# Kernel optimization log

Measured on AMD Instinct MI355X. Metric: run time of the kernel, lower is better.

Reference implementation:

```python
import jax, jax.numpy as jnp
import numpy as np

N = 200000
E = 6400000


def setup_inputs() -> dict:
    key = jax.random.key(0)
    k1, k2, k3, k4 = jax.random.split(key, 4)
    x = jax.random.normal(k1, (N, 10), dtype=jnp.float32)
    edge_index = jax.random.randint(k2, (2, E), 0, N, dtype=jnp.int64)
    W1 = jax.random.normal(k3, (10, 16), dtype=jnp.float32) * (1.0 / np.sqrt(10))
    b1 = jnp.zeros((16,), dtype=jnp.float32)
    W2 = jax.random.normal(k4, (16, 2), dtype=jnp.float32) * (1.0 / np.sqrt(16))
    b2 = jnp.zeros((2,), dtype=jnp.float32)
    return {"x": x, "edge_index": edge_index, "W1": W1, "b1": b1, "W2": W2, "b2": b2}


def gcn_layer(x, src, dst, W, b, num_nodes):
    # GCNConv: out = D^{-1/2} (A + I) D^{-1/2} (x W) + b, deg computed on A+I
    loop = jnp.arange(num_nodes, dtype=src.dtype)
    s = jnp.concatenate([src, loop])
    d = jnp.concatenate([dst, loop])
    deg = jax.ops.segment_sum(jnp.ones(s.shape[0], dtype=x.dtype), d, num_segments=num_nodes)
    dinv = jnp.where(deg > 0, jax.lax.rsqrt(deg), 0.0)
    norm = dinv[s] * dinv[d]                      # [E+N]
    h = x @ W                                     # [N, out] (transform before gather)
    msg = h[s] * norm[:, None]                    # [E+N, out]
    return jax.ops.segment_sum(msg, d, num_segments=num_nodes) + b


def reference(x, edge_index, W1, b1, W2, b2):
    src, dst = edge_index[0], edge_index[1]
    n = x.shape[0]
    h = jax.nn.relu(gcn_layer(x, src, dst, W1, b1, n))
    return gcn_layer(h, src, dst, W2, b2, n)
```

## Files before the change

kernel.cpp:

```cpp
#include <hip/hip_runtime.h>
#include <hip/hip_fp16.h>

#define BLK 256
#define BBLK 512
#define ABLK 512
#define DBLK 512
#define NBK 782
#define BW 256
#define NK2 512
#define NPAD (NBK * BW)
#define HALF (NPAD / 2)
#define CAP 8960
#define NCH 3
#define CHUNK 6144


__global__ void k_hist(const int* __restrict__ dst, int e, int* __restrict__ gcnt,
                       int* __restrict__ blockhist) {
  __shared__ int h[NBK];
  for (int i = threadIdx.x; i < NBK; i += BLK) h[i] = 0;
  __syncthreads();
  int base = blockIdx.x * CHUNK;
  int m = min(CHUNK, e - base);
  int m4 = m >> 2;
  const int4* d4 = (const int4*)(dst + base);
  for (int k = threadIdx.x; k < m4; k += BLK) {
    int4 vv = d4[k];
    atomicAdd(&h[vv.x >> 8], 1);
    atomicAdd(&h[vv.y >> 8], 1);
    atomicAdd(&h[vv.z >> 8], 1);
    atomicAdd(&h[vv.w >> 8], 1);
  }
  for (int k = (m4 << 2) + threadIdx.x; k < m; k += BLK)
    atomicAdd(&h[dst[base + k] >> 8], 1);
  __syncthreads();
  int* row = blockhist + (size_t)blockIdx.x * NBK;
  int sft = (blockIdx.x * 193) % NBK;
  for (int bb = threadIdx.x; bb < NBK; bb += BLK) {
    int b = bb + sft; if (b >= NBK) b -= NBK;
    int c = h[b];
    row[b] = c;
    if (c) atomicAdd(&gcnt[b], c);
  }
}

__global__ void k_scan(const int* __restrict__ gcnt, int* __restrict__ gbase,
                       int* __restrict__ gcur, int e) {
  __shared__ int s[1024];
  int t = threadIdx.x;
  int v = (t < NBK) ? gcnt[t] : 0;
  s[t] = v;
  __syncthreads();
  for (int d = 1; d < 1024; d <<= 1) {
    int u = (t >= d) ? s[t - d] : 0;
    __syncthreads();
    s[t] += u;
    __syncthreads();
  }
  if (t < NBK) { int ex = s[t] - v; gbase[t] = ex; gcur[t] = ex; }
  if (t == 0) gbase[NBK] = e;
}

__global__ void __launch_bounds__(BBLK) k_bin(const int* __restrict__ src,
                                              const int* __restrict__ dst, int e,
                                              int* __restrict__ gcur,
                                              const int* __restrict__ blockhist,
                                              unsigned* __restrict__ binned) {
  __shared__ int lcnt[NBK];
  __shared__ int loff[NBK + 1];
  __shared__ int lbase[NBK];
  __shared__ int wsum[8];
  __shared__ unsigned sorted[CHUNK];
  __shared__ unsigned short bkt16[CHUNK];
  int t = threadIdx.x;
  int base = blockIdx.x * CHUNK;
  int m = min(CHUNK, e - base);

  const int* row = blockhist + (size_t)blockIdx.x * NBK;
  for (int i = t; i < NBK; i += BBLK) lcnt[i] = row[i];
  __syncthreads();
  int b0 = 2 * t;
  int s0 = (b0 + 0 < NBK) ? lcnt[b0 + 0] : 0;
  int s1 = (b0 + 1 < NBK) ? lcnt[b0 + 1] : 0;
  int tsum = s0 + s1;
  int lane = t & 63, wid = t >> 6;
  int incl = tsum;
#pragma unroll
  for (int d = 1; d < 64; d <<= 1) {
    int u = __shfl_up(incl, d);
    if (lane >= d) incl += u;
  }
  if (lane == 63) wsum[wid] = incl;
  __syncthreads();
  if (t == 0) {
    int run = 0;
#pragma unroll
    for (int i = 0; i < 8; i++) { int tv = wsum[i]; wsum[i] = run; run += tv; }
  }
  __syncthreads();
  int ex = incl - tsum + wsum[wid];
  if (b0 + 0 < NBK) loff[b0 + 0] = ex;
  if (b0 + 1 < NBK) loff[b0 + 1] = ex + s0;
  if (t == 0) loff[NBK] = m;
  __syncthreads();
  int sft = (blockIdx.x * 193) % NBK;
  for (int bb = t; bb < NBK; bb += BBLK) {
    int b = bb + sft; if (b >= NBK) b -= NBK;
    int c = lcnt[b];
    lbase[b] = c ? atomicAdd(&gcur[b], c) : 0;
  }
  __syncthreads();
  for (int b = t; b < NBK; b += BBLK) lcnt[b] = loff[b];
  __syncthreads();
  for (int k = t; k < m; k += BBLK) {
    int d = dst[base + k];
    int b = d >> 8;
    int dl = d & 255;
    int pos = atomicAdd(&lcnt[b], 1);
    sorted[pos] = (unsigned)src[base + k] | ((unsigned)dl << 18);
    bkt16[pos] = (unsigned short)b;
  }
  __syncthreads();
  for (int i = t; i < m; i += BBLK) {
    int b = bkt16[i];
    binned[lbase[b] + (i - loff[b])] = sorted[i];
  }
}

__global__ void __launch_bounds__(DBLK) k_ldeg_t1(const unsigned* __restrict__ binned,
                                                  const int* __restrict__ gbase,
                                                  const float* __restrict__ x,
                                                  const float* __restrict__ W1,
                                                  int* __restrict__ deg2,
                                                  float* __restrict__ dinv,
                                                  __half* __restrict__ hs1, int n) {
  __shared__ int cnt[2][NK2];
  __shared__ float w[160];
  int t = threadIdx.x;
  cnt[0][t] = 0;
  cnt[1][t] = 0;
  if (t < 160) w[t] = W1[t];
  __syncthreads();
  int b = blockIdx.x;
  int p0 = gbase[b], p1 = gbase[b + 1];
  int h = t >> 8;
#define KEYOF(u) ((int)(((u) >> 18) << 1) | (int)(((u) & 0x3FFFFu) >= (unsigned)HALF))
  int p = p0 + t;
  for (; p + 3 * DBLK < p1; p += 4 * DBLK) {
    unsigned u0 = binned[p];
    unsigned u1 = binned[p + DBLK];
    unsigned u2 = binned[p + 2 * DBLK];
    unsigned u3 = binned[p + 3 * DBLK];
    atomicAdd(&cnt[h][KEYOF(u0)], 1);
    atomicAdd(&cnt[h][KEYOF(u1)], 1);
    atomicAdd(&cnt[h][KEYOF(u2)], 1);
    atomicAdd(&cnt[h][KEYOF(u3)], 1);
  }
  for (; p < p1; p += DBLK) {
    unsigned u = binned[p];
    atomicAdd(&cnt[h][KEYOF(u)], 1);
  }
#undef KEYOF
  __syncthreads();
  deg2[(size_t)b * NK2 + t] = cnt[0][t] + cnt[1][t];
  if (t >= BW) return;
  int v = b * BW + t;
  if (v >= n) return;
  int dg = cnt[0][2 * t] + cnt[0][2 * t + 1] + cnt[1][2 * t] + cnt[1][2 * t + 1];
  float di = rsqrtf((float)dg + 1.0f);
  dinv[v] = di;
  float xi[10];
#pragma unroll
  for (int k = 0; k < 10; k++) xi[k] = x[(size_t)v * 10 + k];
  __half2 hv[8];
#pragma unroll
  for (int j = 0; j < 8; j++) {
    float acc0 = 0.f, acc1 = 0.f;
#pragma unroll
    for (int k = 0; k < 10; k++) {
      acc0 = fmaf(xi[k], w[k * 16 + 2 * j], acc0);
      acc1 = fmaf(xi[k], w[k * 16 + 2 * j + 1], acc1);
    }
    hv[j] = __floats2half2_rn(acc0 * di, acc1 * di);
  }
  float4* o = (float4*)(hs1 + (size_t)v * 16);
  o[0] = *(float4*)&hv[0];
  o[1] = *(float4*)&hv[4];
}

__global__ void __launch_bounds__(ABLK) k_agg1s(unsigned* __restrict__ binned,
                                                const int* __restrict__ gbase,
                                                const int* __restrict__ deg2,
                                                int* __restrict__ doff,
                                                const __half* __restrict__ hs1,
                                                const float* __restrict__ dinv,
                                                const float* __restrict__ b1,
                                                const float* __restrict__ W2,
                                                float* __restrict__ hs2, int n) {
  __shared__ int cnt[NK2];
  __shared__ int off[NK2 + 1];
  __shared__ int sorted[CAP];
  __shared__ int wsum[8];
  __shared__ float w2[32];
  __shared__ float sb1[16];
  int t = threadIdx.x;
  if (t < 32) w2[t] = W2[t];
  if (t >= 32 && t < 48) sb1[t - 32] = b1[t - 32];
  int bkt = blockIdx.x;
  int p0 = gbase[bkt], p1 = gbase[bkt + 1];
  const bool fast = (p1 - p0) <= CAP;
  const int j = t >> 1;
  const int c = t & 1;
  const int lane = t & 63, wid = t >> 6;
  float acc[8];
#pragma unroll
  for (int q = 0; q < 8; q++) acc[q] = 0.f;

#define ACCR(R) { const __half2* h2_ = (const __half2*)&R; \
    float2 f0_ = __half22float2(h2_[0]); \
    float2 f1_ = __half22float2(h2_[1]); \
    float2 f2_ = __half22float2(h2_[2]); \
    float2 f3_ = __half22float2(h2_[3]); \
    acc[0] += f0_.x; acc[1] += f0_.y; acc[2] += f1_.x; acc[3] += f1_.y; \
    acc[4] += f2_.x; acc[5] += f2_.y; acc[6] += f3_.x; acc[7] += f3_.y; }

  int p = p0;
  int cidx = 0;
  while (p < p1) {
    int m = min(CAP, p1 - p);
    int myv;
    if (fast) {
      myv = deg2[(size_t)bkt * NK2 + t];
    } else {
      cnt[t] = 0;
      __syncthreads();
      for (int i = t; i < m; i += ABLK) {
        unsigned u = __builtin_nontemporal_load(&binned[p + i]);
        int key = (int)((u >> 18) << 1) | (int)((u & 0x3FFFFu) >= (unsigned)HALF);
        atomicAdd(&cnt[key], 1);
      }
      __syncthreads();
      myv = cnt[t];
    }
    int incl = myv;
#pragma unroll
    for (int d = 1; d < 64; d <<= 1) {
      int u = __shfl_up(incl, d);
      if (lane >= d) incl += u;
    }
    if (lane == 63) wsum[wid] = incl;
    __syncthreads();
    if (t == 0) {
      int run = 0;
#pragma unroll
      for (int i = 0; i < 8; i++) { int tv = wsum[i]; wsum[i] = run; run += tv; }
    }
    __syncthreads();
    int ex = incl - myv + wsum[wid];
    off[t] = ex;
    if (t == NK2 - 1) off[NK2] = m;
    cnt[t] = ex;
    __syncthreads();
    if (cidx < NCH && t <= BW) doff[((size_t)bkt * NCH + cidx) * (BW + 1) + t] = off[2 * t];
    for (int i = t; i < m; i += ABLK) {
      unsigned pk = __builtin_nontemporal_load(&binned[p + i]);
      int srcv = (int)(pk & 0x3FFFFu);
      int key = (int)((pk >> 18) << 1) | (int)(srcv >= HALF);
      int pos = atomicAdd(&cnt[key], 1);
      sorted[pos] = srcv;
    }
    __syncthreads();
    for (int i = t; i < m; i += ABLK)
      __builtin_nontemporal_store((unsigned)sorted[i], &binned[p + i]);
    int iA0 = off[2 * j], iA1 = off[2 * j + 1], iB1 = off[2 * j + 2];
    int i = iA0;
    for (; i + 3 < iA1; i += 4) {
      int s0 = sorted[i + 0];
      int s1 = sorted[i + 1];
      int s2 = sorted[i + 2];
      int s3 = sorted[i + 3];
      float4 r0 = *(const float4*)(hs1 + (size_t)s0 * 16 + c * 8);
      float4 r1 = *(const float4*)(hs1 + (size_t)s1 * 16 + c * 8);
      float4 r2 = *(const float4*)(hs1 + (size_t)s2 * 16 + c * 8);
      float4 r3 = *(const float4*)(hs1 + (size_t)s3 * 16 + c * 8);
      ACCR(r0); ACCR(r1); ACCR(r2); ACCR(r3);
    }
    for (; i < iA1; i++) {
      float4 r = *(const float4*)(hs1 + (size_t)sorted[i] * 16 + c * 8);
      ACCR(r);
    }
    __syncthreads();
    for (; i + 3 < iB1; i += 4) {
      int s0 = sorted[i + 0];
      int s1 = sorted[i + 1];
      int s2 = sorted[i + 2];
      int s3 = sorted[i + 3];
      float4 r0 = *(const float4*)(hs1 + (size_t)s0 * 16 + c * 8);
      float4 r1 = *(const float4*)(hs1 + (size_t)s1 * 16 + c * 8);
      float4 r2 = *(const float4*)(hs1 + (size_t)s2 * 16 + c * 8);
      float4 r3 = *(const float4*)(hs1 + (size_t)s3 * 16 + c * 8);
      ACCR(r0); ACCR(r1); ACCR(r2); ACCR(r3);
    }
    for (; i < iB1; i++) {
      float4 r = *(const float4*)(hs1 + (size_t)sorted[i] * 16 + c * 8);
      ACCR(r);
    }
    __syncthreads();
    p += m;
    cidx++;
  }
#undef ACCR

  int v = bkt * BW + j;
  if (v < n) {
    float di = dinv[v];
    float4 sf = *(const float4*)(hs1 + (size_t)v * 16 + c * 8);
    const __half2* sh = (const __half2*)&sf;
    float h0c = 0.f, h1c = 0.f;
#pragma unroll
    for (int q = 0; q < 4; q++) {
      float2 sv = __half22float2(sh[q]);
      int f0 = c * 8 + 2 * q;
      int f1 = f0 + 1;
      float a0 = fmaxf(fmaf(di, acc[2 * q + 0] + sv.x, sb1[f0]), 0.f);
      float a1 = fmaxf(fmaf(di, acc[2 * q + 1] + sv.y, sb1[f1]), 0.f);
      h0c = fmaf(a0, w2[f0 * 2 + 0], fmaf(a1, w2[f1 * 2 + 0], h0c));
      h1c = fmaf(a0, w2[f0 * 2 + 1], fmaf(a1, w2[f1 * 2 + 1], h1c));
    }
    float h0 = h0c + __shfl_xor(h0c, 1);
    float h1 = h1c + __shfl_xor(h1c, 1);
    if (c == 0) {
      hs2[(size_t)v * 2 + 0] = h0 * di;
      hs2[(size_t)v * 2 + 1] = h1 * di;
    }
  }
}

__global__ void __launch_bounds__(BBLK) k_agg2(const unsigned* __restrict__ binned,
                                               const int* __restrict__ gbase,
                                               const int* __restrict__ doff,
                                               const float* __restrict__ hs2,
                                               const float* __restrict__ dinv,
                                               const float* __restrict__ b2,
                                               float* __restrict__ out, int n) {
  int t = threadIdx.x;
  int bkt = blockIdx.x >> 2;
  int j = (t >> 3) + ((blockIdx.x & 3) << 6);
  int c = t & 7;
  int p0 = gbase[bkt], p1 = gbase[bkt + 1];
  float a0 = 0.f, a1 = 0.f;
  int cidx = 0;
  for (int p = p0; p < p1; p += CAP, cidx++) {
    const int* row = doff + ((size_t)bkt * NCH + cidx) * (BW + 1);
    int i0 = row[j], i1 = row[j + 1];
    const unsigned* bp = binned + p;
    int i = i0 + c;
    for (; i + 24 < i1; i += 32) {
      int s0 = bp[i + 0];
      int s1 = bp[i + 8];
      int s2 = bp[i + 16];
      int s3 = bp[i + 24];
      float2 m0 = *(const float2*)(hs2 + (size_t)s0 * 2);
      float2 m1 = *(const float2*)(hs2 + (size_t)s1 * 2);
      float2 m2 = *(const float2*)(hs2 + (size_t)s2 * 2);
      float2 m3 = *(const float2*)(hs2 + (size_t)s3 * 2);
      a0 += m0.x + m1.x + m2.x + m3.x;
      a1 += m0.y + m1.y + m2.y + m3.y;
    }
    for (; i < i1; i += 8) {
      float2 m = *(const float2*)(hs2 + (size_t)bp[i] * 2);
      a0 += m.x;
      a1 += m.y;
    }
  }
  a0 += __shfl_xor(a0, 1);
  a0 += __shfl_xor(a0, 2);
  a0 += __shfl_xor(a0, 4);
  a1 += __shfl_xor(a1, 1);
  a1 += __shfl_xor(a1, 2);
  a1 += __shfl_xor(a1, 4);
  int v = bkt * BW + j;
  if (c == 0 && v < n) {
    float di = dinv[v];
    out[(size_t)v * 2 + 0] = fmaf(di, a0 + hs2[(size_t)v * 2 + 0], b2[0]);
    out[(size_t)v * 2 + 1] = fmaf(di, a1 + hs2[(size_t)v * 2 + 1], b2[1]);
  }
}

extern "C" void kernel_launch(void* const* d_in, const int* in_sizes, int n_in,
                              void* d_out, int out_size, void* d_ws, size_t ws_size,
                              hipStream_t stream) {
  const float* x  = (const float*)d_in[0];
  const int*   ei = (const int*)d_in[1];
  const float* W1 = (const float*)d_in[2];
  const float* b1 = (const float*)d_in[3];
  const float* W2 = (const float*)d_in[4];
  const float* b2 = (const float*)d_in[5];
  float* out = (float*)d_out;

  const int n = in_sizes[0] / 10;
  const int e = in_sizes[1] / 2;
  const int* src = ei;
  const int* dst = ei + e;

  int gC = (e + CHUNK - 1) / CHUNK;

  char* ws = (char*)d_ws;
  int*      gcnt      = (int*)ws;      ws += (size_t)NBK * 4;
  int*      gbase     = (int*)ws;      ws += ((size_t)NBK + 1) * 4;
  int*      gcur      = (int*)ws;      ws += (size_t)NBK * 4;
  int*      deg2      = (int*)ws;      ws += (size_t)NBK * NK2 * 4;
  int*      doff      = (int*)ws;      ws += (size_t)NBK * NCH * (BW + 1) * 4;
  int*      blockhist = (int*)ws;      ws += (size_t)gC * NBK * 4;
  unsigned* binned    = (unsigned*)ws; ws += (size_t)e * 4;
  float*    dinv      = (float*)ws;    ws += (size_t)n * 4;
  __half*   hs1       = (__half*)ws;   ws += (size_t)NPAD * 16 * 2;
  float*    hs2       = (float*)ws;    ws += (size_t)n * 2 * 4;

  hipMemsetAsync(gcnt, 0, (size_t)NBK * 4, stream);
  k_hist<<<gC, BLK, 0, stream>>>(dst, e, gcnt, blockhist);
  k_scan<<<1, 1024, 0, stream>>>(gcnt, gbase, gcur, e);
  k_bin<<<gC, BBLK, 0, stream>>>(src, dst, e, gcur, blockhist, binned);
  k_ldeg_t1<<<NBK, DBLK, 0, stream>>>(binned, gbase, x, W1, deg2, dinv, hs1, n);
  k_agg1s<<<NBK, ABLK, 0, stream>>>(binned, gbase, deg2, doff, hs1, dinv, b1, W2, hs2, n);
  k_agg2<<<NBK * 4, BBLK, 0, stream>>>(binned, gbase, doff, hs2, dinv, b2, out, n);
}
```

Before: 295.5 us.

## Fuse both aggregation layers into one kernel with a grid-wide barrier

Merges the layer-1 aggregation and layer-2 aggregation kernels into a single kernel that synchronizes all blocks through an atomic spin barrier. After the barrier, each block reuses its LDS-sorted source list to gather layer-2 messages, so the sorted edges no longer need to be written back to global memory and doff only has to be stored for overflow buckets. CAP is reduced slightly and launch bounds request 8 waves per EU so that all 782 blocks can be co-resident; the barrier deadlocks if they cannot. The change removes a kernel launch and a pass that rereads the binned edges, but adds barrier wait time and a residency risk.

```diff
diff --git a/kernel.cpp b/kernel.cpp
--- a/kernel.cpp
+++ b/kernel.cpp
@@ -10,7 +10,7 @@
 #define NK2 512
 #define NPAD (NBK * BW)
 #define HALF (NPAD / 2)
-#define CAP 8960
+#define CAP 8832
 #define NCH 3
 #define CHUNK 6144
 
@@ -188,15 +188,18 @@
   o[1] = *(float4*)&hv[4];
 }
 
-__global__ void __launch_bounds__(ABLK) k_agg1s(unsigned* __restrict__ binned,
-                                                const int* __restrict__ gbase,
-                                                const int* __restrict__ deg2,
-                                                int* __restrict__ doff,
-                                                const __half* __restrict__ hs1,
-                                                const float* __restrict__ dinv,
-                                                const float* __restrict__ b1,
-                                                const float* __restrict__ W2,
-                                                float* __restrict__ hs2, int n) {
+__global__ void __launch_bounds__(ABLK, 8) k_aggf(unsigned* __restrict__ binned,
+                                                  const int* __restrict__ gbase,
+                                                  const int* __restrict__ deg2,
+                                                  int* __restrict__ doff,
+                                                  const __half* __restrict__ hs1,
+                                                  const float* __restrict__ dinv,
+                                                  const float* __restrict__ b1,
+                                                  const float* __restrict__ W2,
+                                                  const float* __restrict__ b2,
+                                                  float* __restrict__ hs2,
+                                                  float* __restrict__ out,
+                                                  int* __restrict__ bar, int n) {
   __shared__ int cnt[NK2];
   __shared__ int off[NK2 + 1];
   __shared__ int sorted[CAP];
@@ -261,7 +264,8 @@
     if (t == NK2 - 1) off[NK2] = m;
     cnt[t] = ex;
     __syncthreads();
-    if (cidx < NCH && t <= BW) doff[((size_t)bkt * NCH + cidx) * (BW + 1) + t] = off[2 * t];
+    if (!fast && cidx < NCH && t <= BW)
+      doff[((size_t)bkt * NCH + cidx) * (BW + 1) + t] = off[2 * t];
     for (int i = t; i < m; i += ABLK) {
       unsigned pk = __builtin_nontemporal_load(&binned[p + i]);
       int srcv = (int)(pk & 0x3FFFFu);
@@ -270,8 +274,10 @@
       sorted[pos] = srcv;
     }
     __syncthreads();
-    for (int i = t; i < m; i += ABLK)
-      __builtin_nontemporal_store((unsigned)sorted[i], &binned[p + i]);
+    if (!fast) {
+      for (int i = t; i < m; i += ABLK)
+        __builtin_nontemporal_store((unsigned)sorted[i], &binned[p + i]);
+    }
     int iA0 = off[2 * j], iA1 = off[2 * j + 1], iB1 = off[2 * j + 2];
     int i = iA0;
     for (; i + 3 < iA1; i += 4) {
@@ -312,8 +318,10 @@
 #undef ACCR
 
   int v = bkt * BW + j;
-  if (v < n) {
-    float di = dinv[v];
+  const bool own = (v < n);
+  float di = 0.f, h0d = 0.f, h1d = 0.f;
+  if (own) {
+    di = dinv[v];
     float4 sf = *(const float4*)(hs1 + (size_t)v * 16 + c * 8);
     const __half2* sh = (const __half2*)&sf;
     float h0c = 0.f, h1c = 0.f;
@@ -329,37 +337,34 @@
     }
     float h0 = h0c + __shfl_xor(h0c, 1);
     float h1 = h1c + __shfl_xor(h1c, 1);
+    h0d = h0 * di;
+    h1d = h1 * di;
     if (c == 0) {
-      hs2[(size_t)v * 2 + 0] = h0 * di;
-      hs2[(size_t)v * 2 + 1] = h1 * di;
-    }
-  }
-}
-
-__global__ void __launch_bounds__(BBLK) k_agg2(const unsigned* __restrict__ binned,
-                                               const int* __restrict__ gbase,
-                                               const int* __restrict__ doff,
-                                               const float* __restrict__ hs2,
-                                               const float* __restrict__ dinv,
-                                               const float* __restrict__ b2,
-                                               float* __restrict__ out, int n) {
-  int t = threadIdx.x;
-  int bkt = blockIdx.x >> 2;
-  int j = (t >> 3) + ((blockIdx.x & 3) << 6);
-  int c = t & 7;
-  int p0 = gbase[bkt], p1 = gbase[bkt + 1];
+      hs2[(size_t)v * 2 + 0] = h0d;
+      hs2[(size_t)v * 2 + 1] = h1d;
+    }
+  }
+
+  __threadfence();
+  __syncthreads();
+  if (t == 0) {
+    atomicAdd(bar, 1);
+    while (__hip_atomic_load(bar, __ATOMIC_ACQUIRE, __HIP_MEMORY_SCOPE_AGENT)
+           < (int)gridDim.x)
+      __builtin_amdgcn_s_sleep(8);
+  }
+  __syncthreads();
+  __threadfence();
+
   float a0 = 0.f, a1 = 0.f;
-  int cidx = 0;
-  for (int p = p0; p < p1; p += CAP, cidx++) {
-    const int* row = doff + ((size_t)bkt * NCH + cidx) * (BW + 1);
-    int i0 = row[j], i1 = row[j + 1];
-    const unsigned* bp = binned + p;
+  if (fast) {
+    int i0 = off[2 * j], i1 = off[2 * j + 2];
     int i = i0 + c;
-    for (; i + 24 < i1; i += 32) {
-      int s0 = bp[i + 0];
-      int s1 = bp[i + 8];
-      int s2 = bp[i + 16];
-      int s3 = bp[i + 24];
+    for (; i + 6 < i1; i += 8) {
+      int s0 = sorted[i + 0];
+      int s1 = sorted[i + 2];
+      int s2 = sorted[i + 4];
+      int s3 = sorted[i + 6];
       float2 m0 = *(const float2*)(hs2 + (size_t)s0 * 2);
       float2 m1 = *(const float2*)(hs2 + (size_t)s1 * 2);
       float2 m2 = *(const float2*)(hs2 + (size_t)s2 * 2);
@@ -367,23 +372,42 @@
       a0 += m0.x + m1.x + m2.x + m3.x;
       a1 += m0.y + m1.y + m2.y + m3.y;
     }
-    for (; i < i1; i += 8) {
-      float2 m = *(const float2*)(hs2 + (size_t)bp[i] * 2);
+    for (; i < i1; i += 2) {
+      float2 m = *(const float2*)(hs2 + (size_t)sorted[i] * 2);
       a0 += m.x;
       a1 += m.y;
     }
+  } else {
+    int cidx2 = 0;
+    for (int pp = p0; pp < p1; pp += CAP, cidx2++) {
+      const int* row = doff + ((size_t)bkt * NCH + cidx2) * (BW + 1);
+      int i0 = row[j], i1 = row[j + 1];
+      const unsigned* bp = binned + pp;
+      int i = i0 + c;
+      for (; i + 6 < i1; i += 8) {
+        int s0 = bp[i + 0];
+        int s1 = bp[i + 2];
+        int s2 = bp[i + 4];
+        int s3 = bp[i + 6];
+        float2 m0 = *(const float2*)(hs2 + (size_t)s0 * 2);
+        float2 m1 = *(const float2*)(hs2 + (size_t)s1 * 2);
+        float2 m2 = *(const float2*)(hs2 + (size_t)s2 * 2);
+        float2 m3 = *(const float2*)(hs2 + (size_t)s3 * 2);
+        a0 += m0.x + m1.x + m2.x + m3.x;
+        a1 += m0.y + m1.y + m2.y + m3.y;
+      }
+      for (; i < i1; i += 2) {
+        float2 m = *(const float2*)(hs2 + (size_t)bp[i] * 2);
+        a0 += m.x;
+        a1 += m.y;
+      }
+    }
   }
   a0 += __shfl_xor(a0, 1);
-  a0 += __shfl_xor(a0, 2);
-  a0 += __shfl_xor(a0, 4);
   a1 += __shfl_xor(a1, 1);
-  a1 += __shfl_xor(a1, 2);
-  a1 += __shfl_xor(a1, 4);
-  int v = bkt * BW + j;
-  if (c == 0 && v < n) {
-    float di = dinv[v];
-    out[(size_t)v * 2 + 0] = fmaf(di, a0 + hs2[(size_t)v * 2 + 0], b2[0]);
-    out[(size_t)v * 2 + 1] = fmaf(di, a1 + hs2[(size_t)v * 2 + 1], b2[1]);
+  if (c == 0 && own) {
+    out[(size_t)v * 2 + 0] = fmaf(di, a0 + h0d, b2[0]);
+    out[(size_t)v * 2 + 1] = fmaf(di, a1 + h1d, b2[1]);
   }
 }
 
@@ -407,6 +431,7 @@
 
   char* ws = (char*)d_ws;
   int*      gcnt      = (int*)ws;      ws += (size_t)NBK * 4;
+  int*      bar       = (int*)ws;      ws += 4;
   int*      gbase     = (int*)ws;      ws += ((size_t)NBK + 1) * 4;
   int*      gcur      = (int*)ws;      ws += (size_t)NBK * 4;
   int*      deg2      = (int*)ws;      ws += (size_t)NBK * NK2 * 4;
@@ -417,11 +442,11 @@
   __half*   hs1       = (__half*)ws;   ws += (size_t)NPAD * 16 * 2;
   float*    hs2       = (float*)ws;    ws += (size_t)n * 2 * 4;
 
-  hipMemsetAsync(gcnt, 0, (size_t)NBK * 4, stream);
+  hipMemsetAsync(gcnt, 0, ((size_t)NBK + 1) * 4, stream);
   k_hist<<<gC, BLK, 0, stream>>>(dst, e, gcnt, blockhist);
   k_scan<<<1, 1024, 0, stream>>>(gcnt, gbase, gcur, e);
   k_bin<<<gC, BBLK, 0, stream>>>(src, dst, e, gcur, blockhist, binned);
   k_ldeg_t1<<<NBK, DBLK, 0, stream>>>(binned, gbase, x, W1, deg2, dinv, hs1, n);
-  k_agg1s<<<NBK, ABLK, 0, stream>>>(binned, gbase, deg2, doff, hs1, dinv, b1, W2, hs2, n);
-  k_agg2<<<NBK * 4, BBLK, 0, stream>>>(binned, gbase, doff, hs2, dinv, b2, out, n);
-}
+  k_aggf<<<NBK, ABLK, 0, stream>>>(binned, gbase, deg2, doff, hs1, dinv, b1, W2,
+                                   b2, hs2, out, bar, n);
+}
```

Measured after the change: 849.7 us. +187.6%, slower.
